# Kernel tuning notes

Measured on AMD Instinct MI355X. Metric: run time of the kernel, lower is better.

The kernel has to match this reference:

```python
import jax, jax.numpy as jnp
import numpy as np

N, E, B = 50000, 300000, 64   # nodes, directed edges, graphs
LAT = 4                        # config['latent_size']
EXT = LAT + 4                  # node feature dim (dims 0:2 = xy position)
H = EXT * 64                   # 512 hidden channels
D = EXT * 3 + 6 * H            # combined_readout dim = 3096


def setup_inputs():
    key = jax.random.key(0)
    ks = jax.random.split(key, 20)
    def w(k, fin, fout):
        return jax.random.normal(k, (fin, fout), jnp.float32) / np.float32(np.sqrt(fin))
    z = lambda n: jnp.zeros((n,), jnp.float32)
    return dict(
        x=jax.random.normal(ks[0], (N, EXT), jnp.float32),
        edge_index=jax.random.randint(ks[1], (2, E), 0, N),
        batch_vector=jnp.sort(jax.random.randint(ks[2], (N,), 0, B)),
        target_pos=jax.random.normal(ks[3], (B, 2), jnp.float32),
        W1=w(ks[4], EXT, H), b1=z(H),
        W2=w(ks[5], H, H), b2=z(H),
        W3=w(ks[6], H, H), b3=z(H),
        ph1_w=w(ks[7], 2 + D, 3 * H), ph1_b=z(3 * H),
        ph2_w=w(ks[8], 3 * H, 3 * H), ph2_b=z(3 * H),
        pos_w=w(ks[9], 3 * H, 2), pos_b=z(2),
        vh1_w=w(ks[10], 2 + D, H), vh1_b=z(H),
        vh2_w=w(ks[11], H, H), vh2_b=z(H),
        vec_w=w(ks[12], H, LAT), vec_b=z(LAT),
        sh1_w=w(ks[13], 2 + LAT + D, H), sh1_b=z(H),
        sh2_w=w(ks[14], H, H), sh2_b=z(H),
        sc_w=w(ks[15], H, 1), sc_b=z(1),
        rh1_w=w(ks[16], 2 + LAT + D, H), rh1_b=z(H),
        rh2_w=w(ks[17], H, H), rh2_b=z(H),
        rot_w=w(ks[18], H, 1), rot_b=z(1),
    )


def _forward(x, target_pos, params, edge_index, batch_vector):
    (W1, b1, W2, b2, W3, b3, ph1_w, ph1_b, ph2_w, ph2_b, pos_w, pos_b,
     vh1_w, vh1_b, vh2_w, vh2_b, vec_w, vec_b, sh1_w, sh1_b, sh2_w, sh2_b,
     sc_w, sc_b, rh1_w, rh1_b, rh2_w, rh2_b, rot_w, rot_b) = params
    src, dst = edge_index[0], edge_index[1]
    # PyG gcn_norm with added self-loops: deg[i] = in_degree(i) + 1
    deg = jax.ops.segment_sum(jnp.ones((E,), x.dtype), dst, num_segments=N) + 1.0
    dis = jax.lax.rsqrt(deg)                # D^{-1/2}
    self_norm = (dis * dis)[:, None]        # self-loop coefficient 1/deg[i]

    def gcn(h, W, b):
        h = h @ W
        # norm factorizes: out[i] = dis[i] * sum_{j->i} dis[j]*h[j]  (+ self loop)
        hs = h * dis[:, None]
        agg = jax.ops.segment_sum(hs[src], dst, num_segments=N) * dis[:, None]
        return agg + h * self_norm + b

    counts = jax.ops.segment_sum(jnp.ones((N,), jnp.int32), batch_vector, num_segments=B)
    counts_f = counts.astype(x.dtype)

    def readout(h):  # [global_mean_pool || global_add_pool]
        s = jax.ops.segment_sum(h, batch_vector, num_segments=B)
        return jnp.concatenate([s / counts_f[:, None], s], axis=-1)

    # arrange_face: per graph, 2 nodes with smallest ||pos||, flatten, zero-pad to EXT*3
    lengths = jnp.linalg.norm(x[:, :2], axis=1)
    perm = jnp.lexsort((lengths, batch_vector))   # primary: graph id, secondary: length
    xs = x[perm]
    starts = jnp.cumsum(counts) - counts          # first node of each graph (counts>=2 whp)
    face = jnp.concatenate([xs[starts], xs[starts + 1]], axis=-1)   # [B, 2*EXT]
    face = jnp.pad(face, ((0, 0), (0, EXT * 3 - 2 * EXT)))          # [B, 3*EXT]

    h = jax.nn.relu(gcn(x, W1, b1)); r1 = readout(h)
    h = jax.nn.relu(gcn(h, W2, b2)); r2 = readout(h)
    h = jax.nn.relu(gcn(h, W3, b3)); r3 = readout(h)
    comb = jnp.concatenate([face, r1, r2, r3], axis=-1)             # [B, D]

    pos = jax.nn.relu(jnp.concatenate([target_pos, comb], -1) @ ph1_w + ph1_b)
    pos = jax.nn.relu(pos @ ph2_w + ph2_b)
    pos = pos @ pos_w + pos_b
    vec = jax.nn.relu(jnp.concatenate([pos, comb], -1) @ vh1_w + vh1_b)
    vec = jax.nn.relu(vec @ vh2_w + vh2_b)
    vec = vec @ vec_w + vec_b
    pvc = jnp.concatenate([pos, vec, comb], -1)
    scale = jax.nn.relu(pvc @ sh1_w + sh1_b)
    scale = jax.nn.relu(scale @ sh2_w + sh2_b)
    scale = scale @ sc_w + sc_b
    rot = jax.nn.relu(pvc @ rh1_w + rh1_b)
    rot = jax.nn.relu(rot @ rh2_w + rh2_b)
    rot = rot @ rot_w + rot_b
    return jnp.concatenate([pos, scale, rot, vec], -1).reshape(-1)  # [B*(4+LAT)]


def reference(x, edge_index, batch_vector, target_pos, W1, b1, W2, b2, W3, b3,
              ph1_w, ph1_b, ph2_w, ph2_b, pos_w, pos_b,
              vh1_w, vh1_b, vh2_w, vh2_b, vec_w, vec_b,
              sh1_w, sh1_b, sh2_w, sh2_b, sc_w, sc_b,
              rh1_w, rh1_b, rh2_w, rh2_b, rot_w, rot_b):
    params = (W1, b1, W2, b2, W3, b3, ph1_w, ph1_b, ph2_w, ph2_b, pos_w, pos_b,
              vh1_w, vh1_b, vh2_w, vh2_b, vec_w, vec_b, sh1_w, sh1_b, sh2_w, sh2_b,
              sc_w, sc_b, rh1_w, rh1_b, rh2_w, rh2_b, rot_w, rot_b)
    return _forward(x, target_pos, params, edge_index, batch_vector)
```

## Files before the change

kernel.cpp:

```cpp
#include <hip/hip_runtime.h>
#include <hip/hip_bf16.h>

#define NN 50000
#define NE 300000
#define NBATCH 64
#define HC 512
#define DC 3096

typedef unsigned int u32;
typedef unsigned long long u64;

__global__ void k_deg(const int* __restrict__ ei, int* __restrict__ degc){
  int e = blockIdx.x*256 + threadIdx.x;
  if (e < NE) atomicAdd(&degc[ei[NE + e]], 1);
}
__global__ void k_gcnt(const int* __restrict__ batch, int* __restrict__ gcnt){
  int i = blockIdx.x*256 + threadIdx.x;
  if (i < NN) atomicAdd(&gcnt[batch[i]], 1);
}
__global__ void k_dis(const int* __restrict__ degc, float* __restrict__ dis){
  int i = blockIdx.x*256 + threadIdx.x;
  if (i < NN) dis[i] = rsqrtf((float)degc[i] + 1.0f);
}
__global__ __launch_bounds__(1024) void k_scan(const int* __restrict__ cnt, int* __restrict__ rowp){
  const int CH = (NN + 1023)/1024;
  int lid = threadIdx.x;
  int begin = lid*CH;
  int s = 0;
  for (int j=0;j<CH;j++){ int i=begin+j; if (i<NN) s += cnt[i]; }
  __shared__ int buf[1024];
  buf[lid] = s; __syncthreads();
  for (int off=1; off<1024; off<<=1){
    int t = (lid>=off)? buf[lid-off] : 0; __syncthreads();
    buf[lid] += t; __syncthreads();
  }
  int run = buf[lid] - s;
  for (int j=0;j<CH;j++){ int i=begin+j; if (i<NN){ rowp[i]=run; run += cnt[i]; } }
  if (lid==1023) rowp[NN] = buf[1023];
}
__global__ void k_gstart(const int* __restrict__ gcnt, int* __restrict__ gstart){
  int b = threadIdx.x;
  if (b < NBATCH){ int s=0; for (int j=0;j<b;j++) s += gcnt[j]; gstart[b]=s; }
}
__global__ void k_fill(const int* __restrict__ ei, const int* __restrict__ rowp,
                       int* __restrict__ cursor, int* __restrict__ col){
  int e = blockIdx.x*256 + threadIdx.x;
  if (e < NE){
    int d = ei[NE + e];
    int p = atomicAdd(&cursor[d], 1);
    col[rowp[d] + p] = ei[e];
  }
}

__global__ void k_face1(const float* __restrict__ x, const int* __restrict__ batch, u64* __restrict__ key1){
  int i = blockIdx.x*256 + threadIdx.x;
  if (i >= NN) return;
  float x0 = x[i*8+0], x1 = x[i*8+1];
  float len = sqrtf(x0*x0 + x1*x1);
  u64 key = ((u64)__float_as_uint(len) << 32) | (u32)i;
  atomicMin(&key1[batch[i]], key);
}
__global__ void k_face2(const float* __restrict__ x, const int* __restrict__ batch,
                        const u64* __restrict__ key1, u64* __restrict__ key2){
  int i = blockIdx.x*256 + threadIdx.x;
  if (i >= NN) return;
  int b = batch[i];
  if ((u32)(key1[b] & 0xffffffffu) == (u32)i) return;
  float x0 = x[i*8+0], x1 = x[i*8+1];
  float len = sqrtf(x0*x0 + x1*x1);
  u64 key = ((u64)__float_as_uint(len) << 32) | (u32)i;
  atomicMin(&key2[b], key);
}
__global__ void k_face3(const float* __restrict__ x, const u64* __restrict__ key1,
                        const u64* __restrict__ key2, float* __restrict__ comb){
  int b = threadIdx.x;
  if (b >= NBATCH) return;
  u32 i1 = (u32)(key1[b] & 0xffffffffu);
  u32 i2 = (u32)(key2[b] & 0xffffffffu);
  float* row = comb + (size_t)b*DC;
  for (int j=0;j<8;j++){
    row[j]      = x[(size_t)i1*8 + j];
    row[8 + j]  = x[(size_t)i2*8 + j];
    row[16 + j] = 0.f;
  }
}

__global__ __launch_bounds__(256) void k_gemm1(const float* __restrict__ x, const float* __restrict__ W1,
                                               float* __restrict__ h2){
  int g = blockIdx.x*256 + threadIdx.x;
  if (g >= NN*HC) return;
  int i = g >> 9, c = g & 511;
  const float4* xp = (const float4*)(x + (size_t)i*8);
  float4 x0 = xp[0], x1 = xp[1];
  float acc = 0.f;
  acc = fmaf(x0.x, W1[0*HC + c], acc);
  acc = fmaf(x0.y, W1[1*HC + c], acc);
  acc = fmaf(x0.z, W1[2*HC + c], acc);
  acc = fmaf(x0.w, W1[3*HC + c], acc);
  acc = fmaf(x1.x, W1[4*HC + c], acc);
  acc = fmaf(x1.y, W1[5*HC + c], acc);
  acc = fmaf(x1.z, W1[6*HC + c], acc);
  acc = fmaf(x1.w, W1[7*HC + c], acc);
  h2[g] = acc;
}

__global__ __launch_bounds__(256) void gemm_nk(const float* __restrict__ A, const float* __restrict__ W,
                                               float* __restrict__ C, int M){
  __shared__ float As[16][132];
  __shared__ float Ws[16][132];
  const int tid = threadIdx.x;
  const int r0 = blockIdx.x*128, c0 = blockIdx.y*128;
  const int tx = tid & 15, ty = tid >> 4;
  float acc[8][8];
  #pragma unroll
  for (int i=0;i<8;i++)
    #pragma unroll
    for (int j=0;j<8;j++) acc[i][j]=0.f;
  for (int k0=0; k0<512; k0+=16){
    {
      int m = tid >> 1, kk = (tid & 1)*8;
      int row = r0 + m;
      float4 v0 = make_float4(0,0,0,0), v1 = make_float4(0,0,0,0);
      if (row < M){
        const float4* p = (const float4*)(A + (size_t)row*512 + k0 + kk);
        v0 = p[0]; v1 = p[1];
      }
      As[kk+0][m]=v0.x; As[kk+1][m]=v0.y; As[kk+2][m]=v0.z; As[kk+3][m]=v0.w;
      As[kk+4][m]=v1.x; As[kk+5][m]=v1.y; As[kk+6][m]=v1.z; As[kk+7][m]=v1.w;
    }
    {
      int k = tid >> 4, c = (tid & 15)*8;
      const float4* p = (const float4*)(W + (size_t)(k0 + k)*512 + c0 + c);
      float4 w0 = p[0], w1 = p[1];
      *(float4*)&Ws[k][c]   = w0;
      *(float4*)&Ws[k][c+4] = w1;
    }
    __syncthreads();
    #pragma unroll
    for (int k=0;k<16;k++){
      float a[8], b[8];
      #pragma unroll
      for (int i=0;i<8;i++) a[i] = As[k][ty*8 + i];
      #pragma unroll
      for (int j=0;j<8;j++) b[j] = Ws[k][tx*8 + j];
      #pragma unroll
      for (int i=0;i<8;i++)
        #pragma unroll
        for (int j=0;j<8;j++) acc[i][j] = fmaf(a[i], b[j], acc[i][j]);
    }
    __syncthreads();
  }
  #pragma unroll
  for (int i=0;i<8;i++){
    int row = r0 + ty*8 + i;
    if (row < M){
      float4* q = (float4*)(C + (size_t)row*512 + c0 + tx*8);
      q[0] = make_float4(acc[i][0],acc[i][1],acc[i][2],acc[i][3]);
      q[1] = make_float4(acc[i][4],acc[i][5],acc[i][6],acc[i][7]);
    }
  }
}

__global__ __launch_bounds__(256) void k_agg(const float* __restrict__ h2, const float* __restrict__ dis,
    const int* __restrict__ rowp, const int* __restrict__ col, const float* __restrict__ bias,
    float* __restrict__ act){
  int node = blockIdx.x*4 + (threadIdx.x >> 6);
  if (node >= NN) return;
  int lane = threadIdx.x & 63;
  int c0 = lane*8;
  float acc[8] = {0,0,0,0,0,0,0,0};
  int e0 = rowp[node], e1 = rowp[node+1];
  for (int e=e0; e<e1; e++){
    int j = col[e];
    float dj = dis[j];
    const float4* p = (const float4*)(h2 + (size_t)j*HC + c0);
    float4 v0 = p[0], v1 = p[1];
    acc[0]=fmaf(dj,v0.x,acc[0]); acc[1]=fmaf(dj,v0.y,acc[1]);
    acc[2]=fmaf(dj,v0.z,acc[2]); acc[3]=fmaf(dj,v0.w,acc[3]);
    acc[4]=fmaf(dj,v1.x,acc[4]); acc[5]=fmaf(dj,v1.y,acc[5]);
    acc[6]=fmaf(dj,v1.z,acc[6]); acc[7]=fmaf(dj,v1.w,acc[7]);
  }
  float di = dis[node];
  float sn = di*di;
  const float4* hp = (const float4*)(h2 + (size_t)node*HC + c0);
  float4 h0 = hp[0], h1 = hp[1];
  const float4* bp = (const float4*)(bias + c0);
  float4 b0 = bp[0], b1v = bp[1];
  float o[8];
  o[0]=fmaf(di,acc[0], fmaf(sn,h0.x, b0.x));
  o[1]=fmaf(di,acc[1], fmaf(sn,h0.y, b0.y));
  o[2]=fmaf(di,acc[2], fmaf(sn,h0.z, b0.z));
  o[3]=fmaf(di,acc[3], fmaf(sn,h0.w, b0.w));
  o[4]=fmaf(di,acc[4], fmaf(sn,h1.x, b1v.x));
  o[5]=fmaf(di,acc[5], fmaf(sn,h1.y, b1v.y));
  o[6]=fmaf(di,acc[6], fmaf(sn,h1.z, b1v.z));
  o[7]=fmaf(di,acc[7], fmaf(sn,h1.w, b1v.w));
  #pragma unroll
  for (int i=0;i<8;i++) o[i] = fmaxf(o[i], 0.f);
  float4* q = (float4*)(act + (size_t)node*HC + c0);
  q[0] = make_float4(o[0],o[1],o[2],o[3]);
  q[1] = make_float4(o[4],o[5],o[6],o[7]);
}

__global__ __launch_bounds__(256) void k_readout(const float* __restrict__ act, const int* __restrict__ gstart,
                                                 const int* __restrict__ gcnt, float* __restrict__ gsum){
  int b = blockIdx.x >> 2, part = blockIdx.x & 3;
  int start = gstart[b], cnt = gcnt[b];
  int c = threadIdx.x;
  float a0=0.f, a1=0.f;
  for (int r=part; r<cnt; r+=4){
    const float* row = act + (size_t)(start + r)*HC;
    a0 += row[c]; a1 += row[c + 256];
  }
  atomicAdd(&gsum[b*HC + c], a0);
  atomicAdd(&gsum[b*HC + c + 256], a1);
}
__global__ void k_readout_write(const float* __restrict__ gsum, const int* __restrict__ gcnt,
                                float* __restrict__ comb, int l){
  int g = blockIdx.x*256 + threadIdx.x;
  if (g >= NBATCH*HC) return;
  int b = g >> 9, c = g & 511;
  float s = gsum[g];
  float* row = comb + (size_t)b*DC + 24 + l*1024;
  row[c] = s / (float)gcnt[b];
  row[512 + c] = s;
}

__global__ void k_in0(const float* __restrict__ tp, const float* __restrict__ comb, float* __restrict__ dst){
  int g = blockIdx.x*256 + threadIdx.x;
  if (g >= NBATCH*3098) return;
  int b = g / 3098, c = g - b*3098;
  dst[g] = (c < 2) ? tp[b*2 + c] : comb[(size_t)b*DC + c - 2];
}
__global__ void k_inv(const float* __restrict__ pos, const float* __restrict__ comb, float* __restrict__ dst){
  int g = blockIdx.x*256 + threadIdx.x;
  if (g >= NBATCH*3098) return;
  int b = g / 3098, c = g - b*3098;
  dst[g] = (c < 2) ? pos[b*2 + c] : comb[(size_t)b*DC + c - 2];
}
__global__ void k_pvc(const float* __restrict__ pos, const float* __restrict__ vec,
                      const float* __restrict__ comb, float* __restrict__ dst){
  int g = blockIdx.x*256 + threadIdx.x;
  if (g >= NBATCH*3102) return;
  int b = g / 3102, c = g - b*3102;
  float v;
  if (c < 2) v = pos[b*2 + c];
  else if (c < 6) v = vec[b*4 + c - 2];
  else v = comb[(size_t)b*DC + c - 6];
  dst[g] = v;
}

__global__ __launch_bounds__(256) void head_gemm(const float* __restrict__ A, int K,
    const float* __restrict__ W, int Nw, float* __restrict__ out){
  __shared__ float As[32][68];
  __shared__ float Ws[32][68];
  const int tid = threadIdx.x;
  const int c0 = blockIdx.x*64;
  const int k0 = blockIdx.y*800;
  const int kend = min(K, k0 + 800);
  const int tx = tid & 15, ty = tid >> 4;
  float acc[4][4];
  #pragma unroll
  for (int i=0;i<4;i++)
    #pragma unroll
    for (int j=0;j<4;j++) acc[i][j]=0.f;
  for (int kt=k0; kt<kend; kt+=32){
    {
      int m = tid & 63, kk = (tid >> 6)*8;
      #pragma unroll
      for (int j=0;j<8;j++){
        int k = kt + kk + j;
        As[kk+j][m] = (k < kend) ? A[(size_t)m*K + k] : 0.f;
      }
    }
    {
      int kk = tid >> 3, c = (tid & 7)*8;
      float f[8] = {0,0,0,0,0,0,0,0};
      if (kt + kk < kend){
        const float* wp = W + (size_t)(kt + kk)*Nw + c0 + c;
        #pragma unroll
        for (int j=0;j<8;j++) f[j] = wp[j];
      }
      *(float4*)&Ws[kk][c]   = make_float4(f[0],f[1],f[2],f[3]);
      *(float4*)&Ws[kk][c+4] = make_float4(f[4],f[5],f[6],f[7]);
    }
    __syncthreads();
    #pragma unroll
    for (int k=0;k<32;k++){
      float a[4], b[4];
      #pragma unroll
      for (int i=0;i<4;i++) a[i] = As[k][ty*4 + i];
      #pragma unroll
      for (int j=0;j<4;j++) b[j] = Ws[k][tx*4 + j];
      #pragma unroll
      for (int i=0;i<4;i++)
        #pragma unroll
        for (int j=0;j<4;j++) acc[i][j] = fmaf(a[i], b[j], acc[i][j]);
    }
    __syncthreads();
  }
  #pragma unroll
  for (int i=0;i<4;i++)
    #pragma unroll
    for (int j=0;j<4;j++)
      atomicAdd(&out[(size_t)(ty*4 + i)*Nw + c0 + tx*4 + j], acc[i][j]);
}

__global__ void k_bias_relu(float* __restrict__ buf, const float* __restrict__ bias, int Nw, int do_relu){
  int g = blockIdx.x*256 + threadIdx.x;
  if (g >= NBATCH*Nw) return;
  int c = g % Nw;
  float v = buf[g] + bias[c];
  buf[g] = do_relu ? fmaxf(v, 0.f) : v;
}

__global__ void k_tiny(const float* __restrict__ A, int K, const float* __restrict__ W, int Nw,
                       const float* __restrict__ bias, float* __restrict__ out){
  int g = threadIdx.x;
  if (g >= NBATCH*Nw) return;
  int b = g / Nw, c = g - b*Nw;
  float acc = bias[c];
  const float* a = A + (size_t)b*K;
  for (int k=0;k<K;k++) acc = fmaf(a[k], W[(size_t)k*Nw + c], acc);
  out[g] = acc;
}

__global__ void k_final(const float* __restrict__ pos, const float* __restrict__ sc,
                        const float* __restrict__ rot, const float* __restrict__ vec,
                        float* __restrict__ out){
  int g = blockIdx.x*256 + threadIdx.x;
  if (g >= NBATCH*8) return;
  int b = g >> 3, j = g & 7;
  float v;
  if (j < 2) v = pos[b*2 + j];
  else if (j == 2) v = sc[b];
  else if (j == 3) v = rot[b];
  else v = vec[b*4 + j - 4];
  out[g] = v;
}

static inline int cdiv(int a, int b){ return (a + b - 1)/b; }

extern "C" void kernel_launch(void* const* d_in, const int* in_sizes, int n_in,
                              void* d_out, int out_size, void* d_ws, size_t ws_size,
                              hipStream_t stream)
{
  (void)in_sizes; (void)n_in; (void)out_size;
  const float* x   = (const float*)d_in[0];
  const int* ei    = (const int*)d_in[1];
  const int* batch = (const int*)d_in[2];
  const float* tpos= (const float*)d_in[3];
  const float* W1 = (const float*)d_in[4];  const float* b1 = (const float*)d_in[5];
  const float* W2 = (const float*)d_in[6];  const float* b2 = (const float*)d_in[7];
  const float* W3 = (const float*)d_in[8];  const float* b3 = (const float*)d_in[9];
  const float* ph1w = (const float*)d_in[10]; const float* ph1b = (const float*)d_in[11];
  const float* ph2w = (const float*)d_in[12]; const float* ph2b = (const float*)d_in[13];
  const float* posw = (const float*)d_in[14]; const float* posb = (const float*)d_in[15];
  const float* vh1w = (const float*)d_in[16]; const float* vh1b = (const float*)d_in[17];
  const float* vh2w = (const float*)d_in[18]; const float* vh2b = (const float*)d_in[19];
  const float* vecw = (const float*)d_in[20]; const float* vecb = (const float*)d_in[21];
  const float* sh1w = (const float*)d_in[22]; const float* sh1b = (const float*)d_in[23];
  const float* sh2w = (const float*)d_in[24]; const float* sh2b = (const float*)d_in[25];
  const float* scw  = (const float*)d_in[26]; const float* scb  = (const float*)d_in[27];
  const float* rh1w = (const float*)d_in[28]; const float* rh1b = (const float*)d_in[29];
  const float* rh2w = (const float*)d_in[30]; const float* rh2b = (const float*)d_in[31];
  const float* rotw = (const float*)d_in[32]; const float* rotb = (const float*)d_in[33];
  float* out = (float*)d_out;

  char* w = (char*)d_ws;
  size_t off = 0;
  auto alloc = [&](size_t bytes) -> void* {
    void* p = w + off;
    off = (off + bytes + 255) & ~(size_t)255;
    return p;
  };
  float* h2   = (float*)alloc((size_t)NN*HC*4);
  float* act  = (float*)alloc((size_t)NN*HC*4);
  float* dis  = (float*)alloc((size_t)NN*4);
  int* degc   = (int*)alloc((size_t)NN*4);
  int* rowp   = (int*)alloc((size_t)(NN+1)*4);
  int* cursor = (int*)alloc((size_t)NN*4);
  int* col    = (int*)alloc((size_t)NE*4);
  int* gcnt   = (int*)alloc((size_t)NBATCH*4);
  int* gstart = (int*)alloc((size_t)NBATCH*4);
  u64* key1   = (u64*)alloc((size_t)NBATCH*8);
  u64* key2   = (u64*)alloc((size_t)NBATCH*8);
  float* gsum = (float*)alloc((size_t)NBATCH*HC*4);
  float* comb = (float*)alloc((size_t)NBATCH*DC*4);
  float* in0  = (float*)alloc((size_t)NBATCH*3098*4);
  float* t1   = (float*)alloc((size_t)NBATCH*1536*4);
  float* t2   = (float*)alloc((size_t)NBATCH*1536*4);
  float* inv  = (float*)alloc((size_t)NBATCH*3098*4);
  float* u1   = (float*)alloc((size_t)NBATCH*512*4);
  float* u2   = (float*)alloc((size_t)NBATCH*512*4);
  float* pvc  = (float*)alloc((size_t)NBATCH*3102*4);
  float* sb1  = (float*)alloc((size_t)NBATCH*512*4);
  float* sb2  = (float*)alloc((size_t)NBATCH*512*4);
  float* rb1  = (float*)alloc((size_t)NBATCH*512*4);
  float* rb2  = (float*)alloc((size_t)NBATCH*512*4);
  float* poso = (float*)alloc((size_t)NBATCH*2*4);
  float* veco = (float*)alloc((size_t)NBATCH*4*4);
  float* sco  = (float*)alloc((size_t)NBATCH*4);
  float* roto = (float*)alloc((size_t)NBATCH*4);
  if (off > ws_size) return;

  hipMemsetAsync(degc, 0, (size_t)NN*4, stream);
  hipMemsetAsync(cursor, 0, (size_t)NN*4, stream);
  hipMemsetAsync(gcnt, 0, (size_t)NBATCH*4, stream);
  hipMemsetAsync(key1, 0xFF, (size_t)NBATCH*8, stream);
  hipMemsetAsync(key2, 0xFF, (size_t)NBATCH*8, stream);

  k_deg<<<cdiv(NE,256),256,0,stream>>>(ei, degc);
  k_gcnt<<<cdiv(NN,256),256,0,stream>>>(batch, gcnt);
  k_dis<<<cdiv(NN,256),256,0,stream>>>(degc, dis);
  k_scan<<<1,1024,0,stream>>>(degc, rowp);
  k_gstart<<<1,64,0,stream>>>(gcnt, gstart);
  k_fill<<<cdiv(NE,256),256,0,stream>>>(ei, rowp, cursor, col);
  k_face1<<<cdiv(NN,256),256,0,stream>>>(x, batch, key1);
  k_face2<<<cdiv(NN,256),256,0,stream>>>(x, batch, key1, key2);
  k_face3<<<1,64,0,stream>>>(x, key1, key2, comb);

  k_gemm1<<<cdiv(NN*HC,256),256,0,stream>>>(x, W1, h2);
  k_agg<<<cdiv(NN,4),256,0,stream>>>(h2, dis, rowp, col, b1, act);
  hipMemsetAsync(gsum, 0, (size_t)NBATCH*HC*4, stream);
  k_readout<<<NBATCH*4,256,0,stream>>>(act, gstart, gcnt, gsum);
  k_readout_write<<<cdiv(NBATCH*HC,256),256,0,stream>>>(gsum, gcnt, comb, 0);
  gemm_nk<<<dim3(cdiv(NN,128),4),256,0,stream>>>(act, W2, h2, NN);
  k_agg<<<cdiv(NN,4),256,0,stream>>>(h2, dis, rowp, col, b2, act);
  hipMemsetAsync(gsum, 0, (size_t)NBATCH*HC*4, stream);
  k_readout<<<NBATCH*4,256,0,stream>>>(act, gstart, gcnt, gsum);
  k_readout_write<<<cdiv(NBATCH*HC,256),256,0,stream>>>(gsum, gcnt, comb, 1);
  gemm_nk<<<dim3(cdiv(NN,128),4),256,0,stream>>>(act, W3, h2, NN);
  k_agg<<<cdiv(NN,4),256,0,stream>>>(h2, dis, rowp, col, b3, act);
  hipMemsetAsync(gsum, 0, (size_t)NBATCH*HC*4, stream);
  k_readout<<<NBATCH*4,256,0,stream>>>(act, gstart, gcnt, gsum);
  k_readout_write<<<cdiv(NBATCH*HC,256),256,0,stream>>>(gsum, gcnt, comb, 2);

  k_in0<<<cdiv(NBATCH*3098,256),256,0,stream>>>(tpos, comb, in0);
  hipMemsetAsync(t1, 0, (size_t)NBATCH*1536*4, stream);
  head_gemm<<<dim3(1536/64, cdiv(3098,800)),256,0,stream>>>(in0, 3098, ph1w, 1536, t1);
  k_bias_relu<<<cdiv(NBATCH*1536,256),256,0,stream>>>(t1, ph1b, 1536, 1);
  hipMemsetAsync(t2, 0, (size_t)NBATCH*1536*4, stream);
  head_gemm<<<dim3(1536/64, cdiv(1536,800)),256,0,stream>>>(t1, 1536, ph2w, 1536, t2);
  k_bias_relu<<<cdiv(NBATCH*1536,256),256,0,stream>>>(t2, ph2b, 1536, 1);
  k_tiny<<<1,256,0,stream>>>(t2, 1536, posw, 2, posb, poso);

  k_inv<<<cdiv(NBATCH*3098,256),256,0,stream>>>(poso, comb, inv);
  hipMemsetAsync(u1, 0, (size_t)NBATCH*512*4, stream);
  head_gemm<<<dim3(512/64, cdiv(3098,800)),256,0,stream>>>(inv, 3098, vh1w, 512, u1);
  k_bias_relu<<<cdiv(NBATCH*512,256),256,0,stream>>>(u1, vh1b, 512, 1);
  hipMemsetAsync(u2, 0, (size_t)NBATCH*512*4, stream);
  head_gemm<<<dim3(512/64, 1),256,0,stream>>>(u1, 512, vh2w, 512, u2);
  k_bias_relu<<<cdiv(NBATCH*512,256),256,0,stream>>>(u2, vh2b, 512, 1);
  k_tiny<<<1,256,0,stream>>>(u2, 512, vecw, 4, vecb, veco);

  k_pvc<<<cdiv(NBATCH*3102,256),256,0,stream>>>(poso, veco, comb, pvc);

  hipMemsetAsync(sb1, 0, (size_t)NBATCH*512*4, stream);
  head_gemm<<<dim3(512/64, cdiv(3102,800)),256,0,stream>>>(pvc, 3102, sh1w, 512, sb1);
  k_bias_relu<<<cdiv(NBATCH*512,256),256,0,stream>>>(sb1, sh1b, 512, 1);
  hipMemsetAsync(sb2, 0, (size_t)NBATCH*512*4, stream);
  head_gemm<<<dim3(512/64, 1),256,0,stream>>>(sb1, 512, sh2w, 512, sb2);
  k_bias_relu<<<cdiv(NBATCH*512,256),256,0,stream>>>(sb2, sh2b, 512, 1);
  k_tiny<<<1,256,0,stream>>>(sb2, 512, scw, 1, scb, sco);

  hipMemsetAsync(rb1, 0, (size_t)NBATCH*512*4, stream);
  head_gemm<<<dim3(512/64, cdiv(3102,800)),256,0,stream>>>(pvc, 3102, rh1w, 512, rb1);
  k_bias_relu<<<cdiv(NBATCH*512,256),256,0,stream>>>(rb1, rh1b, 512, 1);
  hipMemsetAsync(rb2, 0, (size_t)NBATCH*512*4, stream);
  head_gemm<<<dim3(512/64, 1),256,0,stream>>>(rb1, 512, rh2w, 512, rb2);
  k_bias_relu<<<cdiv(NBATCH*512,256),256,0,stream>>>(rb2, rh2b, 512, 1);
  k_tiny<<<1,256,0,stream>>>(rb2, 512, rotw, 1, rotb, roto);

  k_final<<<cdiv(NBATCH*8,256),256,0,stream>>>(poso, sco, roto, veco, out);
}
```

Measured before the change: 2.812 ms.

## Use bf16 MFMA for GCN layer GEMMs and bf16 activation storage

Result: faster. 2.403 ms (-14.5%).

```diff
diff --git a/kernel.cpp b/kernel.cpp
--- a/kernel.cpp
+++ b/kernel.cpp
@@ -7,8 +7,23 @@
 #define HC 512
 #define DC 3096
 
+typedef unsigned short u16;
 typedef unsigned int u32;
 typedef unsigned long long u64;
+typedef __attribute__((ext_vector_type(8))) short s16x8;
+typedef __attribute__((ext_vector_type(4))) float f32x4;
+
+static __device__ __forceinline__ float bf2f(u16 u){ return __uint_as_float(((u32)u)<<16); }
+static __device__ __forceinline__ u16 f2bf(float f){
+  __hip_bfloat16 h = __float2bfloat16(f);
+  return *reinterpret_cast<u16*>(&h);
+}
+static __device__ __forceinline__ void bf8up(uint4 r, float* f){
+  f[0]=__uint_as_float(r.x<<16); f[1]=__uint_as_float(r.x&0xffff0000u);
+  f[2]=__uint_as_float(r.y<<16); f[3]=__uint_as_float(r.y&0xffff0000u);
+  f[4]=__uint_as_float(r.z<<16); f[5]=__uint_as_float(r.z&0xffff0000u);
+  f[6]=__uint_as_float(r.w<<16); f[7]=__uint_as_float(r.w&0xffff0000u);
+}
 
 __global__ void k_deg(const int* __restrict__ ei, int* __restrict__ degc){
   int e = blockIdx.x*256 + threadIdx.x;
@@ -86,7 +101,7 @@
 }
 
 __global__ __launch_bounds__(256) void k_gemm1(const float* __restrict__ x, const float* __restrict__ W1,
-                                               float* __restrict__ h2){
+                                               u16* __restrict__ h2){
   int g = blockIdx.x*256 + threadIdx.x;
   if (g >= NN*HC) return;
   int i = g >> 9, c = g & 511;
@@ -101,69 +116,60 @@
   acc = fmaf(x1.y, W1[5*HC + c], acc);
   acc = fmaf(x1.z, W1[6*HC + c], acc);
   acc = fmaf(x1.w, W1[7*HC + c], acc);
-  h2[g] = acc;
-}
-
-__global__ __launch_bounds__(256) void gemm_nk(const float* __restrict__ A, const float* __restrict__ W,
-                                               float* __restrict__ C, int M){
-  __shared__ float As[16][132];
-  __shared__ float Ws[16][132];
-  const int tid = threadIdx.x;
-  const int r0 = blockIdx.x*128, c0 = blockIdx.y*128;
-  const int tx = tid & 15, ty = tid >> 4;
-  float acc[8][8];
-  #pragma unroll
-  for (int i=0;i<8;i++)
-    #pragma unroll
-    for (int j=0;j<8;j++) acc[i][j]=0.f;
-  for (int k0=0; k0<512; k0+=16){
-    {
-      int m = tid >> 1, kk = (tid & 1)*8;
-      int row = r0 + m;
-      float4 v0 = make_float4(0,0,0,0), v1 = make_float4(0,0,0,0);
-      if (row < M){
-        const float4* p = (const float4*)(A + (size_t)row*512 + k0 + kk);
-        v0 = p[0]; v1 = p[1];
-      }
-      As[kk+0][m]=v0.x; As[kk+1][m]=v0.y; As[kk+2][m]=v0.z; As[kk+3][m]=v0.w;
-      As[kk+4][m]=v1.x; As[kk+5][m]=v1.y; As[kk+6][m]=v1.z; As[kk+7][m]=v1.w;
-    }
-    {
-      int k = tid >> 4, c = (tid & 15)*8;
-      const float4* p = (const float4*)(W + (size_t)(k0 + k)*512 + c0 + c);
-      float4 w0 = p[0], w1 = p[1];
-      *(float4*)&Ws[k][c]   = w0;
-      *(float4*)&Ws[k][c+4] = w1;
-    }
-    __syncthreads();
-    #pragma unroll
-    for (int k=0;k<16;k++){
-      float a[8], b[8];
-      #pragma unroll
-      for (int i=0;i<8;i++) a[i] = As[k][ty*8 + i];
-      #pragma unroll
-      for (int j=0;j<8;j++) b[j] = Ws[k][tx*8 + j];
-      #pragma unroll
-      for (int i=0;i<8;i++)
-        #pragma unroll
-        for (int j=0;j<8;j++) acc[i][j] = fmaf(a[i], b[j], acc[i][j]);
-    }
-    __syncthreads();
-  }
-  #pragma unroll
-  for (int i=0;i<8;i++){
-    int row = r0 + ty*8 + i;
-    if (row < M){
-      float4* q = (float4*)(C + (size_t)row*512 + c0 + tx*8);
-      q[0] = make_float4(acc[i][0],acc[i][1],acc[i][2],acc[i][3]);
-      q[1] = make_float4(acc[i][4],acc[i][5],acc[i][6],acc[i][7]);
-    }
-  }
-}
-
-__global__ __launch_bounds__(256) void k_agg(const float* __restrict__ h2, const float* __restrict__ dis,
+  h2[g] = f2bf(acc);
+}
+
+__global__ __launch_bounds__(256) void k_convWT(const float* __restrict__ W, u16* __restrict__ Wt){
+  __shared__ float t[32][33];
+  int n0 = blockIdx.x*32, k0 = blockIdx.y*32;
+  int tx = threadIdx.x & 31, ty = threadIdx.x >> 5;
+  #pragma unroll
+  for (int j=0;j<4;j++)
+    t[ty*4+j][tx] = W[(size_t)(k0 + ty*4 + j)*512 + n0 + tx];
+  __syncthreads();
+  #pragma unroll
+  for (int j=0;j<4;j++)
+    Wt[(size_t)(n0 + ty*4 + j)*512 + k0 + tx] = f2bf(t[tx][ty*4+j]);
+}
+
+__global__ __launch_bounds__(256) void gemm_mfma(const u16* __restrict__ A, const u16* __restrict__ Wt,
+                                                 u16* __restrict__ C, int M){
+  int stripe = blockIdx.x*4 + (threadIdx.x >> 6);
+  if (stripe >= (M >> 4)) return;
+  int lane = threadIdx.x & 63;
+  int r  = lane & 15;
+  int ko = (lane >> 4) * 8;
+  s16x8 a[16];
+  const u16* arow = A + (size_t)(stripe*16 + r)*512 + ko;
+  #pragma unroll
+  for (int kt=0; kt<16; kt++)
+    a[kt] = *(const s16x8*)(arow + kt*32);
+  for (int nt=0; nt<32; nt+=2){
+    const u16* b0 = Wt + (size_t)(nt*16 + r)*512 + ko;
+    const u16* b1 = b0 + 16*512;
+    f32x4 acc0 = {0.f,0.f,0.f,0.f};
+    f32x4 acc1 = {0.f,0.f,0.f,0.f};
+    #pragma unroll
+    for (int kt=0; kt<16; kt++){
+      s16x8 vb0 = *(const s16x8*)(b0 + kt*32);
+      s16x8 vb1 = *(const s16x8*)(b1 + kt*32);
+      acc0 = __builtin_amdgcn_mfma_f32_16x16x32_bf16(a[kt], vb0, acc0, 0, 0, 0);
+      acc1 = __builtin_amdgcn_mfma_f32_16x16x32_bf16(a[kt], vb1, acc1, 0, 0, 0);
+    }
+    int drow = stripe*16 + ((lane >> 4) << 2);
+    u16* cp0 = C + (size_t)drow*512 + nt*16 + r;
+    u16* cp1 = cp0 + 16;
+    #pragma unroll
+    for (int q=0;q<4;q++){
+      cp0[(size_t)q*512] = f2bf(acc0[q]);
+      cp1[(size_t)q*512] = f2bf(acc1[q]);
+    }
+  }
+}
+
+__global__ __launch_bounds__(256) void k_agg(const u16* __restrict__ h2, const float* __restrict__ dis,
     const int* __restrict__ rowp, const int* __restrict__ col, const float* __restrict__ bias,
-    float* __restrict__ act){
+    u16* __restrict__ act){
   int node = blockIdx.x*4 + (threadIdx.x >> 6);
   if (node >= NN) return;
   int lane = threadIdx.x & 63;
@@ -173,44 +179,37 @@
   for (int e=e0; e<e1; e++){
     int j = col[e];
     float dj = dis[j];
-    const float4* p = (const float4*)(h2 + (size_t)j*HC + c0);
-    float4 v0 = p[0], v1 = p[1];
-    acc[0]=fmaf(dj,v0.x,acc[0]); acc[1]=fmaf(dj,v0.y,acc[1]);
-    acc[2]=fmaf(dj,v0.z,acc[2]); acc[3]=fmaf(dj,v0.w,acc[3]);
-    acc[4]=fmaf(dj,v1.x,acc[4]); acc[5]=fmaf(dj,v1.y,acc[5]);
-    acc[6]=fmaf(dj,v1.z,acc[6]); acc[7]=fmaf(dj,v1.w,acc[7]);
+    uint4 raw = *(const uint4*)(h2 + (size_t)j*HC + c0);
+    float v[8]; bf8up(raw, v);
+    #pragma unroll
+    for (int i=0;i<8;i++) acc[i] = fmaf(dj, v[i], acc[i]);
   }
   float di = dis[node];
   float sn = di*di;
-  const float4* hp = (const float4*)(h2 + (size_t)node*HC + c0);
-  float4 h0 = hp[0], h1 = hp[1];
+  uint4 sraw = *(const uint4*)(h2 + (size_t)node*HC + c0);
+  float hs[8]; bf8up(sraw, hs);
   const float4* bp = (const float4*)(bias + c0);
   float4 b0 = bp[0], b1v = bp[1];
-  float o[8];
-  o[0]=fmaf(di,acc[0], fmaf(sn,h0.x, b0.x));
-  o[1]=fmaf(di,acc[1], fmaf(sn,h0.y, b0.y));
-  o[2]=fmaf(di,acc[2], fmaf(sn,h0.z, b0.z));
-  o[3]=fmaf(di,acc[3], fmaf(sn,h0.w, b0.w));
-  o[4]=fmaf(di,acc[4], fmaf(sn,h1.x, b1v.x));
-  o[5]=fmaf(di,acc[5], fmaf(sn,h1.y, b1v.y));
-  o[6]=fmaf(di,acc[6], fmaf(sn,h1.z, b1v.z));
-  o[7]=fmaf(di,acc[7], fmaf(sn,h1.w, b1v.w));
-  #pragma unroll
-  for (int i=0;i<8;i++) o[i] = fmaxf(o[i], 0.f);
-  float4* q = (float4*)(act + (size_t)node*HC + c0);
-  q[0] = make_float4(o[0],o[1],o[2],o[3]);
-  q[1] = make_float4(o[4],o[5],o[6],o[7]);
-}
-
-__global__ __launch_bounds__(256) void k_readout(const float* __restrict__ act, const int* __restrict__ gstart,
+  float bb[8] = {b0.x,b0.y,b0.z,b0.w,b1v.x,b1v.y,b1v.z,b1v.w};
+  u32 ow[4];
+  #pragma unroll
+  for (int i=0;i<4;i++){
+    float o0 = fmaxf(fmaf(di,acc[2*i],   fmaf(sn,hs[2*i],   bb[2*i])),   0.f);
+    float o1 = fmaxf(fmaf(di,acc[2*i+1], fmaf(sn,hs[2*i+1], bb[2*i+1])), 0.f);
+    ow[i] = (u32)f2bf(o0) | ((u32)f2bf(o1) << 16);
+  }
+  *(uint4*)(act + (size_t)node*HC + c0) = make_uint4(ow[0],ow[1],ow[2],ow[3]);
+}
+
+__global__ __launch_bounds__(256) void k_readout(const u16* __restrict__ act, const int* __restrict__ gstart,
                                                  const int* __restrict__ gcnt, float* __restrict__ gsum){
   int b = blockIdx.x >> 2, part = blockIdx.x & 3;
   int start = gstart[b], cnt = gcnt[b];
   int c = threadIdx.x;
   float a0=0.f, a1=0.f;
   for (int r=part; r<cnt; r+=4){
-    const float* row = act + (size_t)(start + r)*HC;
-    a0 += row[c]; a1 += row[c + 256];
+    const u16* row = act + (size_t)(start + r)*HC;
+    a0 += bf2f(row[c]); a1 += bf2f(row[c + 256]);
   }
   atomicAdd(&gsum[b*HC + c], a0);
   atomicAdd(&gsum[b*HC + c + 256], a1);
@@ -304,6 +303,54 @@
     #pragma unroll
     for (int j=0;j<4;j++)
       atomicAdd(&out[(size_t)(ty*4 + i)*Nw + c0 + tx*4 + j], acc[i][j]);
+}
+
+__global__ __launch_bounds__(256) void head_fused512(const float* __restrict__ A,
+    const float* __restrict__ W, const float* __restrict__ bias, float* __restrict__ out){
+  __shared__ float As[32][68];
+  __shared__ float Ws[32][68];
+  const int tid = threadIdx.x;
+  const int c0 = blockIdx.x*64;
+  const int tx = tid & 15, ty = tid >> 4;
+  float acc[4][4];
+  #pragma unroll
+  for (int i=0;i<4;i++)
+    #pragma unroll
+    for (int j=0;j<4;j++) acc[i][j]=0.f;
+  for (int kt=0; kt<512; kt+=32){
+    {
+      int m = tid & 63, kk = (tid >> 6)*8;
+      #pragma unroll
+      for (int j=0;j<8;j++) As[kk+j][m] = A[(size_t)m*512 + kt + kk + j];
+    }
+    {
+      int kk = tid >> 3, c = (tid & 7)*8;
+      const float* wp = W + (size_t)(kt + kk)*512 + c0 + c;
+      #pragma unroll
+      for (int j=0;j<8;j++) Ws[kk][c+j] = wp[j];
+    }
+    __syncthreads();
+    #pragma unroll
+    for (int k=0;k<32;k++){
+      float a[4], b[4];
+      #pragma unroll
+      for (int i=0;i<4;i++) a[i] = As[k][ty*4 + i];
+      #pragma unroll
+      for (int j=0;j<4;j++) b[j] = Ws[k][tx*4 + j];
+      #pragma unroll
+      for (int i=0;i<4;i++)
+        #pragma unroll
+        for (int j=0;j<4;j++) acc[i][j] = fmaf(a[i], b[j], acc[i][j]);
+    }
+    __syncthreads();
+  }
+  #pragma unroll
+  for (int i=0;i<4;i++)
+    #pragma unroll
+    for (int j=0;j<4;j++){
+      int ccol = c0 + tx*4 + j;
+      out[(size_t)(ty*4 + i)*512 + ccol] = fmaxf(acc[i][j] + bias[ccol], 0.f);
+    }
 }
 
 __global__ void k_bias_relu(float* __restrict__ buf, const float* __restrict__ bias, int Nw, int do_relu){
@@ -374,8 +421,10 @@
     off = (off + bytes + 255) & ~(size_t)255;
     return p;
   };
-  float* h2   = (float*)alloc((size_t)NN*HC*4);
-  float* act  = (float*)alloc((size_t)NN*HC*4);
+  u16* h2b    = (u16*)alloc((size_t)NN*HC*2);
+  u16* actb   = (u16*)alloc((size_t)NN*HC*2);
+  u16* Wt2    = (u16*)alloc((size_t)HC*HC*2);
+  u16* Wt3    = (u16*)alloc((size_t)HC*HC*2);
   float* dis  = (float*)alloc((size_t)NN*4);
   int* degc   = (int*)alloc((size_t)NN*4);
   int* rowp   = (int*)alloc((size_t)(NN+1)*4);
@@ -419,21 +468,25 @@
   k_face1<<<cdiv(NN,256),256,0,stream>>>(x, batch, key1);
   k_face2<<<cdiv(NN,256),256,0,stream>>>(x, batch, key1, key2);
   k_face3<<<1,64,0,stream>>>(x, key1, key2, comb);
-
-  k_gemm1<<<cdiv(NN*HC,256),256,0,stream>>>(x, W1, h2);
-  k_agg<<<cdiv(NN,4),256,0,stream>>>(h2, dis, rowp, col, b1, act);
+  k_convWT<<<dim3(16,16),256,0,stream>>>(W2, Wt2);
+  k_convWT<<<dim3(16,16),256,0,stream>>>(W3, Wt3);
+
+  k_gemm1<<<cdiv(NN*HC,256),256,0,stream>>>(x, W1, h2b);
+  k_agg<<<cdiv(NN,4),256,0,stream>>>(h2b, dis, rowp, col, b1, actb);
   hipMemsetAsync(gsum, 0, (size_t)NBATCH*HC*4, stream);
-  k_readout<<<NBATCH*4,256,0,stream>>>(act, gstart, gcnt, gsum);
+  k_readout<<<NBATCH*4,256,0,stream>>>(actb, gstart, gcnt, gsum);
   k_readout_write<<<cdiv(NBATCH*HC,256),256,0,stream>>>(gsum, gcnt, comb, 0);
-  gemm_nk<<<dim3(cdiv(NN,128),4),256,0,stream>>>(act, W2, h2, NN);
-  k_agg<<<cdiv(NN,4),256,0,stream>>>(h2, dis, rowp, col, b2, act);
+
+  gemm_mfma<<<cdiv(NN/16,4),256,0,stream>>>(actb, Wt2, h2b, NN);
+  k_agg<<<cdiv(NN,4),256,0,stream>>>(h2b, dis, rowp, col, b2, actb);
   hipMemsetAsync(gsum, 0, (size_t)NBATCH*HC*4, stream);
-  k_readout<<<NBATCH*4,256,0,stream>>>(act, gstart, gcnt, gsum);
+  k_readout<<<NBATCH*4,256,0,stream>>>(actb, gstart, gcnt, gsum);
   k_readout_write<<<cdiv(NBATCH*HC,256),256,0,stream>>>(gsum, gcnt, comb, 1);
-  gemm_nk<<<dim3(cdiv(NN,128),4),256,0,stream>>>(act, W3, h2, NN);
-  k_agg<<<cdiv(NN,4),256,0,stream>>>(h2, dis, rowp, col, b3, act);
+
+  gemm_mfma<<<cdiv(NN/16,4),256,0,stream>>>(actb, Wt3, h2b, NN);
+  k_agg<<<cdiv(NN,4),256,0,stream>>>(h2b, dis, rowp, col, b3, actb);
   hipMemsetAsync(gsum, 0, (size_t)NBATCH*HC*4, stream);
-  k_readout<<<NBATCH*4,256,0,stream>>>(act, gstart, gcnt, gsum);
+  k_readout<<<NBATCH*4,256,0,stream>>>(actb, gstart, gcnt, gsum);
   k_readout_write<<<cdiv(NBATCH*HC,256),256,0,stream>>>(gsum, gcnt, comb, 2);
 
   k_in0<<<cdiv(NBATCH*3098,256),256,0,stream>>>(tpos, comb, in0);
@@ -449,9 +502,7 @@
   hipMemsetAsync(u1, 0, (size_t)NBATCH*512*4, stream);
   head_gemm<<<dim3(512/64, cdiv(3098,800)),256,0,stream>>>(inv, 3098, vh1w, 512, u1);
   k_bias_relu<<<cdiv(NBATCH*512,256),256,0,stream>>>(u1, vh1b, 512, 1);
-  hipMemsetAsync(u2, 0, (size_t)NBATCH*512*4, stream);
-  head_gemm<<<dim3(512/64, 1),256,0,stream>>>(u1, 512, vh2w, 512, u2);
-  k_bias_relu<<<cdiv(NBATCH*512,256),256,0,stream>>>(u2, vh2b, 512, 1);
+  head_fused512<<<8,256,0,stream>>>(u1, vh2w, vh2b, u2);
   k_tiny<<<1,256,0,stream>>>(u2, 512, vecw, 4, vecb, veco);
 
   k_pvc<<<cdiv(NBATCH*3102,256),256,0,stream>>>(poso, veco, comb, pvc);
@@ -459,17 +510,13 @@
   hipMemsetAsync(sb1, 0, (size_t)NBATCH*512*4, stream);
   head_gemm<<<dim3(512/64, cdiv(3102,800)),256,0,stream>>>(pvc, 3102, sh1w, 512, sb1);
   k_bias_relu<<<cdiv(NBATCH*512,256),256,0,stream>>>(sb1, sh1b, 512, 1);
-  hipMemsetAsync(sb2, 0, (size_t)NBATCH*512*4, stream);
-  head_gemm<<<dim3(512/64, 1),256,0,stream>>>(sb1, 512, sh2w, 512, sb2);
-  k_bias_relu<<<cdiv(NBATCH*512,256),256,0,stream>>>(sb2, sh2b, 512, 1);
+  head_fused512<<<8,256,0,stream>>>(sb1, sh2w, sh2b, sb2);
   k_tiny<<<1,256,0,stream>>>(sb2, 512, scw, 1, scb, sco);
 
   hipMemsetAsync(rb1, 0, (size_t)NBATCH*512*4, stream);
   head_gemm<<<dim3(512/64, cdiv(3102,800)),256,0,stream>>>(pvc, 3102, rh1w, 512, rb1);
   k_bias_relu<<<cdiv(NBATCH*512,256),256,0,stream>>>(rb1, rh1b, 512, 1);
-  hipMemsetAsync(rb2, 0, (size_t)NBATCH*512*4, stream);
-  head_gemm<<<dim3(512/64, 1),256,0,stream>>>(rb1, 512, rh2w, 512, rb2);
-  k_bias_relu<<<cdiv(NBATCH*512,256),256,0,stream>>>(rb2, rh2b, 512, 1);
+  head_fused512<<<8,256,0,stream>>>(rb1, rh2w, rh2b, rb2);
   k_tiny<<<1,256,0,stream>>>(rb2, 512, rotw, 1, rotb, roto);
 
   k_final<<<cdiv(NBATCH*8,256),256,0,stream>>>(poso, sco, roto, veco, out);
```
